# Kernel tuning notes

Measured on AMD Instinct MI355X. Metric: run time of the kernel, lower is better.

## Reference

```python
import jax, jax.numpy as jnp
import numpy as np

EMBD = 16
NUM_NODES = 100000
NUM_EDGES = 3200000
BN_EPS = 1e-5


def setup_inputs() -> dict:
    key = jax.random.key(0)
    ks = jax.random.split(key, 12)
    x = jax.random.normal(ks[0], (NUM_NODES, EMBD), dtype=jnp.float32)
    edge_index = jax.random.randint(ks[1], (2, NUM_EDGES), 0, NUM_NODES, dtype=jnp.int64)
    edge_attr = jax.random.normal(ks[2], (NUM_EDGES, EMBD), dtype=jnp.float32)
    s = 1.0 / np.sqrt(EMBD)  # torch Linear default init scale
    W0 = jax.random.uniform(ks[3], (EMBD, EMBD), jnp.float32, -s, s)
    b0 = jax.random.uniform(ks[4], (EMBD,), jnp.float32, -s, s)
    W1 = jax.random.uniform(ks[5], (EMBD, EMBD), jnp.float32, -s, s)
    b1 = jax.random.uniform(ks[6], (EMBD,), jnp.float32, -s, s)
    W2 = jax.random.uniform(ks[7], (EMBD, EMBD), jnp.float32, -s, s)
    b2 = jax.random.uniform(ks[8], (EMBD,), jnp.float32, -s, s)
    gamma = jnp.ones((EMBD,), jnp.float32)
    beta = jnp.zeros((EMBD,), jnp.float32)
    return {"x": x, "edge_index": edge_index, "edge_attr": edge_attr,
            "W0": W0, "b0": b0, "W1": W1, "b1": b1, "W2": W2, "b2": b2,
            "gamma": gamma, "beta": beta}


def reference(x, edge_index, edge_attr, W0, b0, W1, b1, W2, b2, gamma, beta):
    # Gather source/dest node features per edge: (num_edges, embd)
    h_src = x[edge_index[0]]
    h_dest = x[edge_index[1]]
    # Three small linears (torch Linear: y = x @ W.T + b), summed
    e = (edge_attr @ W0.T + b0) + (h_src @ W1.T + b1) + (h_dest @ W2.T + b2)
    # BatchNorm1d in training mode: biased batch statistics over edge dim
    mean = jnp.mean(e, axis=0)
    var = jnp.var(e, axis=0)  # biased, matches torch normalization
    e = (e - mean) * jax.lax.rsqrt(var + BN_EPS) * gamma + beta
    # ReLU + residual
    return edge_attr + jax.nn.relu(e)
```

## Files before the change

### kernel.cpp

```cpp
#include <hip/hip_runtime.h>
#include <math.h>

#define NN 100000
#define NE 3200000

constexpr int BLK = 256;
constexpr int GRID_E1 = 4096;
constexpr int GRID_E2 = 2048;

typedef float f4 __attribute__((ext_vector_type(4)));
typedef _Float16 h4 __attribute__((ext_vector_type(4)));
typedef _Float16 h8 __attribute__((ext_vector_type(8)));


__device__ __forceinline__ void matvec16_acc(const float* __restrict__ sW,
                                             const float v[16], float acc[16]) {
#pragma unroll
  for (int j = 0; j < 16; ++j) {
    float a = acc[j];
#pragma unroll
    for (int q = 0; q < 4; ++q) {
      float4 w = ((const float4*)(sW + j * 16))[q];
      a = fmaf(v[q * 4 + 0], w.x, a);
      a = fmaf(v[q * 4 + 1], w.y, a);
      a = fmaf(v[q * 4 + 2], w.z, a);
      a = fmaf(v[q * 4 + 3], w.w, a);
    }
    acc[j] = a;
  }
}

__device__ __forceinline__ void load_row16(const float* __restrict__ base,
                                           size_t row, float v[16]) {
  const f4* r = (const f4*)(base + row * 16);
#pragma unroll
  for (int q = 0; q < 4; ++q) {
    f4 t = r[q];
    v[q * 4 + 0] = t[0]; v[q * 4 + 1] = t[1];
    v[q * 4 + 2] = t[2]; v[q * 4 + 3] = t[3];
  }
}

__device__ __forceinline__ void load_row16_nt(const float* __restrict__ base,
                                              size_t row, float v[16]) {
  const f4* r = (const f4*)(base + row * 16);
#pragma unroll
  for (int q = 0; q < 4; ++q) {
    f4 t = __builtin_nontemporal_load(r + q);
    v[q * 4 + 0] = t[0]; v[q * 4 + 1] = t[1];
    v[q * 4 + 2] = t[2]; v[q * 4 + 3] = t[3];
  }
}

__device__ __forceinline__ h8 pack_h8(const float* v) {
  h8 o;
#pragma unroll
  for (int i = 0; i < 8; ++i) o[i] = (_Float16)v[i];
  return o;
}

__global__ __launch_bounds__(BLK)
void node_proj(const float* __restrict__ x, const float* __restrict__ W1,
               const float* __restrict__ W2, h8* __restrict__ p1h,
               h8* __restrict__ p2h, float* __restrict__ stats) {
  __shared__ __align__(16) float sW1[256];
  __shared__ __align__(16) float sW2[256];
  if (blockIdx.x == 0 && threadIdx.x < 32) stats[threadIdx.x] = 0.f;
  for (int i = threadIdx.x; i < 256; i += BLK) { sW1[i] = W1[i]; sW2[i] = W2[i]; }
  __syncthreads();
  int n = blockIdx.x * BLK + threadIdx.x;
  if (n >= NN) return;
  float xv[16];
  load_row16(x, (size_t)n, xv);
  float y1[16], y2[16];
#pragma unroll
  for (int j = 0; j < 16; ++j) { y1[j] = 0.f; y2[j] = 0.f; }
  matvec16_acc(sW1, xv, y1);
  matvec16_acc(sW2, xv, y2);
  p1h[(size_t)n * 2 + 0] = pack_h8(y1);
  p1h[(size_t)n * 2 + 1] = pack_h8(y1 + 8);
  p2h[(size_t)n * 2 + 0] = pack_h8(y2);
  p2h[(size_t)n * 2 + 1] = pack_h8(y2 + 8);
}

__global__ __launch_bounds__(BLK)
void edge_pass1_fast(const float* __restrict__ ea, const int* __restrict__ ei,
                     const h8* __restrict__ p1h, const h8* __restrict__ p2h,
                     const float* __restrict__ W0g, float* __restrict__ stats,
                     _Float16* __restrict__ eh) {
  __shared__ __align__(16) float sW0[256];
  __shared__ float red[4][32];
  for (int i = threadIdx.x; i < 256; i += BLK) sW0[i] = W0g[i];
  __syncthreads();

  float sum[8], ssq[8];
#pragma unroll
  for (int j = 0; j < 8; ++j) { sum[j] = 0.f; ssq[j] = 0.f; }

  const int tid = blockIdx.x * BLK + threadIdx.x;
  const int r = tid & 1;
  const int stride = (GRID_E1 * BLK) >> 1;
  int e = tid >> 1;

  int s = 0, d = 0;
  if (e < NE) {
    s = __builtin_nontemporal_load(ei + e);
    d = __builtin_nontemporal_load(ei + NE + e);
  }
  for (; e < NE; e += stride) {
    int en = e + stride;
    int sn = 0, dn = 0;
    if (en < NE) {
      sn = __builtin_nontemporal_load(ei + en);
      dn = __builtin_nontemporal_load(ei + NE + en);
    }
    const f4* ear = (const f4*)(ea + (size_t)e * 16 + r * 8);
    f4 a0 = __builtin_nontemporal_load(ear + 0);
    f4 a1 = __builtin_nontemporal_load(ear + 1);
    float own[8] = {a0[0], a0[1], a0[2], a0[3], a1[0], a1[1], a1[2], a1[3]};
    float oth[8];
#pragma unroll
    for (int k = 0; k < 8; ++k) oth[k] = __shfl_xor(own[k], 1);
    h8 g1 = p1h[(size_t)s * 2 + r];
    h8 g2 = p2h[(size_t)d * 2 + r];
    float ev[8];
#pragma unroll
    for (int j = 0; j < 8; ++j) ev[j] = (float)g1[j] + (float)g2[j];
    const float* wbase = sW0 + r * 128;
#pragma unroll
    for (int j = 0; j < 8; ++j) {
      const float* wrow = wbase + j * 16;
      const f4* wA = (const f4*)(wrow + r * 8);
      const f4* wB = (const f4*)(wrow + (r ^ 1) * 8);
      float acc = ev[j];
#pragma unroll
      for (int q = 0; q < 2; ++q) {
        f4 w = wA[q];
        acc = fmaf(own[4 * q + 0], w[0], acc);
        acc = fmaf(own[4 * q + 1], w[1], acc);
        acc = fmaf(own[4 * q + 2], w[2], acc);
        acc = fmaf(own[4 * q + 3], w[3], acc);
      }
#pragma unroll
      for (int q = 0; q < 2; ++q) {
        f4 w = wB[q];
        acc = fmaf(oth[4 * q + 0], w[0], acc);
        acc = fmaf(oth[4 * q + 1], w[1], acc);
        acc = fmaf(oth[4 * q + 2], w[2], acc);
        acc = fmaf(oth[4 * q + 3], w[3], acc);
      }
      ev[j] = acc;
    }
#pragma unroll
    for (int j = 0; j < 8; ++j) {
      sum[j] += ev[j];
      ssq[j] = fmaf(ev[j], ev[j], ssq[j]);
    }
    h8* ep = (h8*)(eh + (size_t)e * 16 + r * 8);
    __builtin_nontemporal_store(pack_h8(ev), ep);
    s = sn; d = dn;
  }

#pragma unroll
  for (int off = 32; off >= 2; off >>= 1) {
#pragma unroll
    for (int j = 0; j < 8; ++j) {
      sum[j] += __shfl_down(sum[j], off);
      ssq[j] += __shfl_down(ssq[j], off);
    }
  }
  int wid = threadIdx.x >> 6;
  int lane = threadIdx.x & 63;
  if (lane < 2) {
#pragma unroll
    for (int j = 0; j < 8; ++j) {
      red[wid][lane * 8 + j] = sum[j];
      red[wid][16 + lane * 8 + j] = ssq[j];
    }
  }
  __syncthreads();
  if (threadIdx.x < 32) {
    float v = red[0][threadIdx.x] + red[1][threadIdx.x] +
              red[2][threadIdx.x] + red[3][threadIdx.x];
    atomicAdd(stats + threadIdx.x, v);
  }
}

template <bool TABS, bool EH>
__global__ __launch_bounds__(BLK)
void edge_pass1(const float* __restrict__ ea, const int* __restrict__ ei,
                const float* __restrict__ xO, const h8* __restrict__ p1h,
                const h8* __restrict__ p2h, const float* __restrict__ W0g,
                const float* __restrict__ W1g, const float* __restrict__ W2g,
                float* __restrict__ stats, _Float16* __restrict__ eh,
                float* __restrict__ out) {
  __shared__ __align__(16) float sW0[256];
  __shared__ __align__(16) float sW1[256];
  __shared__ __align__(16) float sW2[256];
  __shared__ float red[4][32];
  for (int i = threadIdx.x; i < 256; i += BLK) {
    sW0[i] = W0g[i];
    if (!TABS) { sW1[i] = W1g[i]; sW2[i] = W2g[i]; }
  }
  __syncthreads();

  float sum[16], ssq[16];
#pragma unroll
  for (int j = 0; j < 16; ++j) { sum[j] = 0.f; ssq[j] = 0.f; }

  const int total = gridDim.x * BLK;
  for (int e = blockIdx.x * BLK + threadIdx.x; e < NE; e += total) {
    int s = __builtin_nontemporal_load(ei + e);
    int d = __builtin_nontemporal_load(ei + NE + e);
    float eav[16];
    load_row16_nt(ea, (size_t)e, eav);
    float ev[16];
    if (TABS) {
      h8 a0 = p1h[(size_t)s * 2 + 0];
      h8 a1 = p1h[(size_t)s * 2 + 1];
      h8 b0 = p2h[(size_t)d * 2 + 0];
      h8 b1 = p2h[(size_t)d * 2 + 1];
#pragma unroll
      for (int j = 0; j < 8; ++j) {
        ev[j]     = (float)a0[j] + (float)b0[j];
        ev[8 + j] = (float)a1[j] + (float)b1[j];
      }
      matvec16_acc(sW0, eav, ev);
    } else {
      float xs[16], xd[16];
      load_row16(xO, (size_t)s, xs);
      load_row16(xO, (size_t)d, xd);
#pragma unroll
      for (int j = 0; j < 16; ++j) ev[j] = 0.f;
      matvec16_acc(sW0, eav, ev);
      matvec16_acc(sW1, xs, ev);
      matvec16_acc(sW2, xd, ev);
    }
#pragma unroll
    for (int j = 0; j < 16; ++j) {
      sum[j] += ev[j];
      ssq[j] = fmaf(ev[j], ev[j], ssq[j]);
    }
    if (EH) {
      h8* ep = (h8*)(eh + (size_t)e * 16);
      __builtin_nontemporal_store(pack_h8(ev), ep);
      __builtin_nontemporal_store(pack_h8(ev + 8), ep + 1);
    } else {
      f4* orow = (f4*)(out + (size_t)e * 16);
#pragma unroll
      for (int q = 0; q < 4; ++q) {
        f4 o;
        o[0] = ev[q * 4 + 0]; o[1] = ev[q * 4 + 1];
        o[2] = ev[q * 4 + 2]; o[3] = ev[q * 4 + 3];
        __builtin_nontemporal_store(o, orow + q);
      }
    }
  }

#pragma unroll
  for (int off = 32; off > 0; off >>= 1) {
#pragma unroll
    for (int j = 0; j < 16; ++j) {
      sum[j] += __shfl_down(sum[j], off);
      ssq[j] += __shfl_down(ssq[j], off);
    }
  }
  int wid = threadIdx.x >> 6;
  int lane = threadIdx.x & 63;
  if (lane == 0) {
#pragma unroll
    for (int j = 0; j < 16; ++j) {
      red[wid][j] = sum[j];
      red[wid][16 + j] = ssq[j];
    }
  }
  __syncthreads();
  if (threadIdx.x < 32) {
    float v = red[0][threadIdx.x] + red[1][threadIdx.x] +
              red[2][threadIdx.x] + red[3][threadIdx.x];
    atomicAdd(stats + threadIdx.x, v);
  }
}

template <bool EH>
__global__ __launch_bounds__(BLK, 8)
void edge_pass2(const float* __restrict__ ea, const _Float16* __restrict__ eh,
                const float* __restrict__ stats, const float* __restrict__ gamma,
                const float* __restrict__ beta, float* __restrict__ out) {
  __shared__ float sSS[32];
  if (threadIdx.x < 16) {
    int j = threadIdx.x;
    const float inv_n = 1.0f / (float)NE;
    float mean = stats[j] * inv_n;
    float var = fmaf(-mean, mean, stats[16 + j] * inv_n);
    float sc = gamma[j] / sqrtf(var + 1e-5f);
    sSS[j] = sc;
    sSS[16 + j] = fmaf(-mean, sc, beta[j]);
  }
  __syncthreads();
  const int totalv = NE * 4;
  const int stride = gridDim.x * BLK;
  int i0 = blockIdx.x * BLK + threadIdx.x;
  int c = (i0 & 3) * 4;
  float sc0 = sSS[c + 0], sc1 = sSS[c + 1], sc2 = sSS[c + 2], sc3 = sSS[c + 3];
  float sh0 = sSS[16 + c + 0], sh1 = sSS[16 + c + 1];
  float sh2 = sSS[16 + c + 2], sh3 = sSS[16 + c + 3];
  for (int i = i0; i < totalv; i += stride) {
    f4 av = __builtin_nontemporal_load((const f4*)ea + i);
    f4 evv;
    if (EH) {
      h4 hv = __builtin_nontemporal_load((const h4*)eh + i);
      evv[0] = (float)hv[0]; evv[1] = (float)hv[1];
      evv[2] = (float)hv[2]; evv[3] = (float)hv[3];
    } else {
      evv = __builtin_nontemporal_load((const f4*)out + i);
    }
    f4 o;
    o[0] = av[0] + fmaxf(0.f, fmaf(evv[0], sc0, sh0));
    o[1] = av[1] + fmaxf(0.f, fmaf(evv[1], sc1, sh1));
    o[2] = av[2] + fmaxf(0.f, fmaf(evv[2], sc2, sh2));
    o[3] = av[3] + fmaxf(0.f, fmaf(evv[3], sc3, sh3));
    __builtin_nontemporal_store(o, (f4*)out + i);
  }
}

extern "C" void kernel_launch(void* const* d_in, const int* in_sizes, int n_in,
                              void* d_out, int out_size, void* d_ws, size_t ws_size,
                              hipStream_t stream) {
  const float* x     = (const float*)d_in[0];
  const int*   ei    = (const int*)d_in[1];
  const float* ea    = (const float*)d_in[2];
  const float* W0    = (const float*)d_in[3];
  const float* W1    = (const float*)d_in[5];
  const float* W2    = (const float*)d_in[7];
  const float* gamma = (const float*)d_in[9];
  const float* beta  = (const float*)d_in[10];
  float* out = (float*)d_out;

  float* stats = (float*)d_ws;
  h8* p1h = (h8*)((char*)d_ws + 1024);
  h8* p2h = p1h + (size_t)NN * 2;
  _Float16* eh = (_Float16*)(p2h + (size_t)NN * 2);

  size_t need_tabs = 1024 + (size_t)NN * 64;
  size_t need_eh   = need_tabs + (size_t)NE * 32;
  bool has_tabs = ws_size >= need_tabs;
  bool has_eh   = ws_size >= need_eh;

  if (has_tabs) {
    node_proj<<<(NN + BLK - 1) / BLK, BLK, 0, stream>>>(x, W1, W2, p1h, p2h, stats);
    if (has_eh)
      edge_pass1_fast<<<GRID_E1, BLK, 0, stream>>>(ea, ei, p1h, p2h, W0, stats, eh);
    else
      edge_pass1<true, false><<<GRID_E2, BLK, 0, stream>>>(
          ea, ei, x, p1h, p2h, W0, W1, W2, stats, eh, out);
  } else {
    hipMemsetAsync(stats, 0, 32 * sizeof(float), stream);
    edge_pass1<false, false><<<GRID_E2, BLK, 0, stream>>>(
        ea, ei, x, p1h, p2h, W0, W1, W2, stats, eh, out);
  }

  if (has_eh)
    edge_pass2<true><<<GRID_E2, BLK, 0, stream>>>(ea, eh, stats, gamma, beta, out);
  else
    edge_pass2<false><<<GRID_E2, BLK, 0, stream>>>(ea, eh, stats, gamma, beta, out);
}
```

Baseline: 507.6 us.

## Software-pipeline edge pass 1 loads two iterations ahead and halve grid

Restructures the grid-stride loop in the first edge pass so that edge indices are prefetched two iterations ahead, and edge attributes plus gathered node projections are prefetched one iteration ahead. The aim is to hide the dependent gather latency (index load, then feature load) behind compute. The grid is halved so each thread runs more iterations, which gives the pipeline more room to work but leaves fewer waves to hide latency. Register pressure also rises from the extra in-flight values.

```diff
diff --git a/kernel.cpp b/kernel.cpp
--- a/kernel.cpp
+++ b/kernel.cpp
@@ -5,7 +5,7 @@
 #define NE 3200000
 
 constexpr int BLK = 256;
-constexpr int GRID_E1 = 4096;
+constexpr int GRID_E1 = 2048;
 constexpr int GRID_E2 = 2048;
 
 typedef float f4 __attribute__((ext_vector_type(4)));
@@ -99,33 +99,55 @@
 
   const int tid = blockIdx.x * BLK + threadIdx.x;
   const int r = tid & 1;
-  const int stride = (GRID_E1 * BLK) >> 1;
+  const int S = (GRID_E1 * BLK) >> 1;
   int e = tid >> 1;
 
-  int s = 0, d = 0;
+  int s1 = 0, d1 = 0;
+  int s2 = 0, d2 = 0;
+  f4 a0c = {}, a1c = {};
+  h8 g1c = {}, g2c = {};
   if (e < NE) {
-    s = __builtin_nontemporal_load(ei + e);
-    d = __builtin_nontemporal_load(ei + NE + e);
-  }
-  for (; e < NE; e += stride) {
-    int en = e + stride;
-    int sn = 0, dn = 0;
+    s1 = ei[e];
+    d1 = ei[NE + e];
+  }
+  if (e + S < NE) {
+    s2 = __builtin_nontemporal_load(ei + e + S);
+    d2 = __builtin_nontemporal_load(ei + NE + e + S);
+  }
+  if (e < NE) {
+    const f4* ear = (const f4*)(ea + (size_t)e * 16 + r * 8);
+    a0c = __builtin_nontemporal_load(ear + 0);
+    a1c = __builtin_nontemporal_load(ear + 1);
+    g1c = p1h[(size_t)s1 * 2 + r];
+    g2c = p2h[(size_t)d1 * 2 + r];
+  }
+
+  f4 a0n = {}, a1n = {};
+  h8 g1n = {}, g2n = {};
+  for (; e < NE; e += S) {
+    const int en = e + S;
+    const int enn = en + S;
     if (en < NE) {
-      sn = __builtin_nontemporal_load(ei + en);
-      dn = __builtin_nontemporal_load(ei + NE + en);
-    }
-    const f4* ear = (const f4*)(ea + (size_t)e * 16 + r * 8);
-    f4 a0 = __builtin_nontemporal_load(ear + 0);
-    f4 a1 = __builtin_nontemporal_load(ear + 1);
-    float own[8] = {a0[0], a0[1], a0[2], a0[3], a1[0], a1[1], a1[2], a1[3]};
+      const f4* earn = (const f4*)(ea + (size_t)en * 16 + r * 8);
+      a0n = __builtin_nontemporal_load(earn + 0);
+      a1n = __builtin_nontemporal_load(earn + 1);
+      g1n = p1h[(size_t)s2 * 2 + r];
+      g2n = p2h[(size_t)d2 * 2 + r];
+    }
+    int s3 = 0, d3 = 0;
+    if (enn < NE) {
+      s3 = __builtin_nontemporal_load(ei + enn);
+      d3 = __builtin_nontemporal_load(ei + NE + enn);
+    }
+
+    float own[8] = {a0c[0], a0c[1], a0c[2], a0c[3],
+                    a1c[0], a1c[1], a1c[2], a1c[3]};
     float oth[8];
 #pragma unroll
     for (int k = 0; k < 8; ++k) oth[k] = __shfl_xor(own[k], 1);
-    h8 g1 = p1h[(size_t)s * 2 + r];
-    h8 g2 = p2h[(size_t)d * 2 + r];
     float ev[8];
 #pragma unroll
-    for (int j = 0; j < 8; ++j) ev[j] = (float)g1[j] + (float)g2[j];
+    for (int j = 0; j < 8; ++j) ev[j] = (float)g1c[j] + (float)g2c[j];
     const float* wbase = sW0 + r * 128;
 #pragma unroll
     for (int j = 0; j < 8; ++j) {
@@ -158,7 +180,9 @@
     }
     h8* ep = (h8*)(eh + (size_t)e * 16 + r * 8);
     __builtin_nontemporal_store(pack_h8(ev), ep);
-    s = sn; d = dn;
+
+    a0c = a0n; a1c = a1n; g1c = g1n; g2c = g2n;
+    s2 = s3; d2 = d3;
   }
 
 #pragma unroll
```

Result: no change. 498.6 us (-1.8%).
